# Performance work log

Hardware: AMD Instinct MI355X
Metric: run time of the kernel (lower is better)

## Reference

```python
import jax, jax.numpy as jnp
import numpy as np

H = 4096          # hidden_size
I = 14336         # intermediate_size
G = 128           # quantization group size along the input dim


def dequant(q, s, g=G):
    """Dequantize group-scaled int4 weights.
    q: [out, in] int (values in [-8, 7]); s: [out, in//g] float scales.
    Returns fp weight [out, in]: W[o, i] = q[o, i] * s[o, i // g].
    """
    O, In = q.shape
    return (q.reshape(O, In // g, g).astype(s.dtype) * s[:, :, None]).reshape(O, In)


def setup_inputs() -> dict:
    key = jax.random.key(0)
    ks = jax.random.split(key, 7)
    x = jax.random.normal(ks[0], (2, 2048, H), dtype=jnp.float32)

    def mk_qlinear(kq, ksc, out_d, in_d):
        q = jax.random.randint(kq, (out_d, in_d), -8, 8, dtype=jnp.int32)  # int4 range
        s = jax.random.uniform(ksc, (out_d, in_d // G), dtype=jnp.float32,
                               minval=0.005, maxval=0.02)
        return q, s

    gate_q, gate_s = mk_qlinear(ks[1], ks[2], I, H)
    up_q, up_s = mk_qlinear(ks[3], ks[4], I, H)
    down_q, down_s = mk_qlinear(ks[5], ks[6], H, I)
    return {"x": x,
            "gate_q": gate_q, "gate_s": gate_s,
            "up_q": up_q, "up_s": up_s,
            "down_q": down_q, "down_s": down_s}


def reference(x, gate_q, gate_s, up_q, up_s, down_q, down_s):
    # SwiGLU MLP: down( silu(gate(x)) * up(x) ) with group-dequantized weights.
    Wg = dequant(gate_q, gate_s)   # [I, H]
    Wu = dequant(up_q, up_s)       # [I, H]
    Wd = dequant(down_q, down_s)   # [H, I]
    gate_score = jax.nn.silu(jnp.einsum('bsh,ih->bsi', x, Wg))
    intermediate = gate_score * jnp.einsum('bsh,ih->bsi', x, Wu)
    return jnp.einsum('bsi,hi->bsh', intermediate, Wd)
```

## Files before the change

### kernel.cpp

```cpp
#include <hip/hip_runtime.h>
#include <hip/hip_bf16.h>


#define HDIM 4096
#define IDIM 14336
#define MTOK 4096
#define GRP 128

typedef __attribute__((ext_vector_type(8))) short bf16x8;
typedef __attribute__((ext_vector_type(4))) float f32x4;
typedef __attribute__((ext_vector_type(4))) unsigned short u16x4;

#define WAIT_LGKM0 asm volatile("s_waitcnt lgkmcnt(0)" ::: "memory")
#define WAIT_VM(N) asm volatile("s_waitcnt vmcnt(" #N ")" ::: "memory")
#define SBAR       __builtin_amdgcn_s_barrier()
#define SCHB       __builtin_amdgcn_sched_barrier(0)

__device__ __forceinline__ unsigned short f2bf(float f) {
  union { float f; unsigned int u; } v; v.f = f;
  return (unsigned short)((v.u + 0x7fffu + ((v.u >> 16) & 1u)) >> 16);
}
__device__ __forceinline__ unsigned pk2(float a, float b) {
  union { float f; unsigned u; } ua, ub; ua.f = a; ub.f = b;
  return __builtin_amdgcn_perm(ub.u, ua.u, 0x07060302u);
}

#define GLD16(G, L)                                                           \
  __builtin_amdgcn_global_load_lds(                                           \
      (const __attribute__((address_space(1))) unsigned int*)(G),             \
      (__attribute__((address_space(3))) unsigned int*)(L), 16, 0, 0)

__global__ __launch_bounds__(256) void cvt_x_kernel(const float* __restrict__ x,
                                                    unsigned short* __restrict__ xb) {
  const int n = MTOK * HDIM;
  const int stride = gridDim.x * 256 * 4;
  for (int i = (blockIdx.x * 256 + threadIdx.x) * 4; i < n; i += stride) {
    float4 v = *reinterpret_cast<const float4*>(x + i);
    u16x4 o;
    o[0] = f2bf(v.x); o[1] = f2bf(v.y); o[2] = f2bf(v.z); o[3] = f2bf(v.w);
    *reinterpret_cast<u16x4*>(xb + i) = o;
  }
}

__global__ __launch_bounds__(256) void deq_kernel(const int* __restrict__ q,
                                                  const float* __restrict__ s,
                                                  unsigned short* __restrict__ w,
                                                  int In) {
  const int row  = blockIdx.y;
  const int col0 = blockIdx.x * 2048 + threadIdx.x * 8;
  const long base = (long)row * In + col0;
  const float sc = s[row * (In / GRP) + (col0 >> 7)];
  const int4* p = (const int4*)(q + base);
  int4 a0 = p[0], a1 = p[1];
  uint4 o;
  o.x = pk2((float)a0.x * sc, (float)a0.y * sc);
  o.y = pk2((float)a0.z * sc, (float)a0.w * sc);
  o.z = pk2((float)a1.x * sc, (float)a1.y * sc);
  o.w = pk2((float)a1.z * sc, (float)a1.w * sc);
  *(uint4*)(w + base) = o;
}

__global__ __launch_bounds__(512, 2) void gateup_bf16(
    const unsigned short* __restrict__ xb,
    const unsigned short* __restrict__ wg,
    const unsigned short* __restrict__ wu,
    unsigned short* __restrict__ inter)
{
  __shared__ unsigned short As[2 * 256 * 64];
  __shared__ unsigned short Bgs[2 * 128 * 64];
  __shared__ unsigned short Bus[2 * 128 * 64];

  const int tid = threadIdx.x, lane = tid & 63, wid = tid >> 6;
  const int wm = wid >> 1, wn = wid & 1;
  const int p = blockIdx.x;
  const int l = (p & 7) * 224 + (p >> 3);
  const int m0 = (l & 15) * 256, n0 = (l >> 4) * 128;
  const int lr = lane & 15, lc = lane >> 4;

  const int ra   = tid >> 3;
  const int scol = ((tid & 7) ^ (ra & 7)) << 3;
  const unsigned short* pa  = xb + (long)(m0 + ra) * HDIM + scol;
  const unsigned short* pbg = wg + (long)(n0 + ra) * HDIM + scol;
  const unsigned short* pbu = wu + (long)(n0 + ra) * HDIM + scol;

#define A1(KT, BUF, IT)                                                       \
  GLD16(pa + (long)(IT) * 64 * HDIM + (long)(KT) * 64,                        \
        (unsigned short*)As + (BUF) * 16384 + (IT) * 4096 + wid * 512)
#define BG1(KT, BUF, IT)                                                      \
  GLD16(pbg + (long)(IT) * 64 * HDIM + (long)(KT) * 64,                       \
        (unsigned short*)Bgs + (BUF) * 8192 + (IT) * 4096 + wid * 512)
#define BU1(KT, BUF, IT)                                                      \
  GLD16(pbu + (long)(IT) * 64 * HDIM + (long)(KT) * 64,                       \
        (unsigned short*)Bus + (BUF) * 8192 + (IT) * 4096 + wid * 512)

  f32x4 accg[4][4], accu[4][4];
  const f32x4 zero = {0.f, 0.f, 0.f, 0.f};
#pragma unroll
  for (int i = 0; i < 4; ++i)
#pragma unroll
    for (int j = 0; j < 4; ++j) { accg[i][j] = zero; accu[i][j] = zero; }

  BG1(0, 0, 0); BG1(0, 0, 1); BU1(0, 0, 0); BU1(0, 0, 1);
  A1(0, 0, 0); A1(0, 0, 1); A1(0, 0, 2); A1(0, 0, 3);
  SCHB;
  WAIT_VM(0);
  SBAR;
  SCHB;

  const int NK = HDIM / 64;
#pragma unroll 1
  for (int kt = 0; kt < NK; ++kt) {
    const int RD = kt & 1, WR = RD ^ 1;
    const int ktn = (kt + 1 < NK) ? kt + 1 : NK - 1;
    const unsigned short* Ab  = (const unsigned short*)As  + RD * 16384;
    const unsigned short* Bgb = (const unsigned short*)Bgs + RD * 8192;
    const unsigned short* Bub = (const unsigned short*)Bus + RD * 8192;
    const int soff0 = (lc ^ (lr & 7)) << 3;
    const int soff1 = ((4 + lc) ^ (lr & 7)) << 3;
    bf16x8 af[4], bg[4], bu[4];

#pragma unroll
    for (int mi = 0; mi < 4; ++mi)
      af[mi] = *(const bf16x8*)&Ab[(wm * 64 + mi * 16 + lr) * 64 + soff0];
#pragma unroll
    for (int ni = 0; ni < 4; ++ni) {
      bg[ni] = *(const bf16x8*)&Bgb[(wn * 64 + ni * 16 + lr) * 64 + soff0];
      bu[ni] = *(const bf16x8*)&Bub[(wn * 64 + ni * 16 + lr) * 64 + soff0];
    }
    BG1(ktn, WR, 0); BG1(ktn, WR, 1); BU1(ktn, WR, 0); BU1(ktn, WR, 1);
    SCHB; WAIT_LGKM0; SCHB;
    __builtin_amdgcn_s_setprio(1);
#pragma unroll
    for (int ni = 0; ni < 4; ++ni)
#pragma unroll
      for (int mi = 0; mi < 4; ++mi) {
        accg[mi][ni] = __builtin_amdgcn_mfma_f32_16x16x32_bf16(af[mi], bg[ni], accg[mi][ni], 0, 0, 0);
        accu[mi][ni] = __builtin_amdgcn_mfma_f32_16x16x32_bf16(af[mi], bu[ni], accu[mi][ni], 0, 0, 0);
      }
    __builtin_amdgcn_s_setprio(0);

#pragma unroll
    for (int mi = 0; mi < 4; ++mi)
      af[mi] = *(const bf16x8*)&Ab[(wm * 64 + mi * 16 + lr) * 64 + soff1];
#pragma unroll
    for (int ni = 0; ni < 4; ++ni) {
      bg[ni] = *(const bf16x8*)&Bgb[(wn * 64 + ni * 16 + lr) * 64 + soff1];
      bu[ni] = *(const bf16x8*)&Bub[(wn * 64 + ni * 16 + lr) * 64 + soff1];
    }
    A1(ktn, WR, 0); A1(ktn, WR, 1); A1(ktn, WR, 2); A1(ktn, WR, 3);
    SCHB; WAIT_LGKM0; SCHB;
    __builtin_amdgcn_s_setprio(1);
#pragma unroll
    for (int ni = 0; ni < 4; ++ni)
#pragma unroll
      for (int mi = 0; mi < 4; ++mi) {
        accg[mi][ni] = __builtin_amdgcn_mfma_f32_16x16x32_bf16(af[mi], bg[ni], accg[mi][ni], 0, 0, 0);
        accu[mi][ni] = __builtin_amdgcn_mfma_f32_16x16x32_bf16(af[mi], bu[ni], accu[mi][ni], 0, 0, 0);
      }
    __builtin_amdgcn_s_setprio(0);

    SCHB;
    WAIT_VM(0);
    SBAR;
    SCHB;
  }

  const int r0 = m0 + wm * 64, c0 = n0 + wn * 64;
#pragma unroll
  for (int mi = 0; mi < 4; ++mi)
#pragma unroll
    for (int ni = 0; ni < 4; ++ni)
#pragma unroll
      for (int r = 0; r < 4; ++r) {
        float g = accg[mi][ni][r], u = accu[mi][ni][r];
        float sv = g / (1.f + __expf(-g));
        int row = r0 + mi * 16 + lc * 4 + r;
        int col = c0 + ni * 16 + lr;
        inter[(long)row * IDIM + col] = f2bf(sv * u);
      }
#undef A1
#undef BG1
#undef BU1
}

__global__ __launch_bounds__(512, 2) void down_bf16(
    const unsigned short* __restrict__ inter,
    const unsigned short* __restrict__ wd,
    float* __restrict__ out)
{
  __shared__ unsigned short As[2 * 256 * 64];
  __shared__ unsigned short Bs[2 * 256 * 64];

  const int tid = threadIdx.x, lane = tid & 63, wid = tid >> 6;
  const int wm = wid >> 2, wn = wid & 3;
  const int p = blockIdx.x;
  const int l = (p & 7) * 32 + (p >> 3);
  const int m0 = (l & 15) * 256, n0 = (l >> 4) * 256;
  const int lr = lane & 15, lc = lane >> 4;

  const int ra   = tid >> 3;
  const int scol = ((tid & 7) ^ (ra & 7)) << 3;
  const unsigned short* pa = inter + (long)(m0 + ra) * IDIM + scol;
  const unsigned short* pb = wd + (long)(n0 + ra) * IDIM + scol;

#define DA1(KT, BUF, IT)                                                      \
  GLD16(pa + (long)(IT) * 64 * IDIM + (long)(KT) * 64,                        \
        (unsigned short*)As + (BUF) * 16384 + (IT) * 4096 + wid * 512)
#define DB1(KT, BUF, IT)                                                      \
  GLD16(pb + (long)(IT) * 64 * IDIM + (long)(KT) * 64,                        \
        (unsigned short*)Bs + (BUF) * 16384 + (IT) * 4096 + wid * 512)

  f32x4 acc[8][4];
  const f32x4 zero = {0.f, 0.f, 0.f, 0.f};
#pragma unroll
  for (int i = 0; i < 8; ++i)
#pragma unroll
    for (int j = 0; j < 4; ++j) acc[i][j] = zero;

  DB1(0, 0, 0); DB1(0, 0, 1); DB1(0, 0, 2); DB1(0, 0, 3);
  DA1(0, 0, 0); DA1(0, 0, 1); DA1(0, 0, 2); DA1(0, 0, 3);
  SCHB;
  WAIT_VM(0);
  SBAR;
  SCHB;

  const int NK = IDIM / 64;
#pragma unroll 1
  for (int kt = 0; kt < NK; ++kt) {
    const int RD = kt & 1, WR = RD ^ 1;
    const int ktn = (kt + 1 < NK) ? kt + 1 : NK - 1;
    const unsigned short* Ab = (const unsigned short*)As + RD * 16384;
    const unsigned short* Bb = (const unsigned short*)Bs + RD * 16384;
    const int soff0 = (lc ^ (lr & 7)) << 3;
    const int soff1 = ((4 + lc) ^ (lr & 7)) << 3;
    bf16x8 af[8], bfr[4];

#pragma unroll
    for (int mi = 0; mi < 8; ++mi)
      af[mi] = *(const bf16x8*)&Ab[(wm * 128 + mi * 16 + lr) * 64 + soff0];
#pragma unroll
    for (int ni = 0; ni < 4; ++ni)
      bfr[ni] = *(const bf16x8*)&Bb[(wn * 64 + ni * 16 + lr) * 64 + soff0];
    DB1(ktn, WR, 0); DB1(ktn, WR, 1); DB1(ktn, WR, 2); DB1(ktn, WR, 3);
    SCHB; WAIT_LGKM0; SCHB;
    __builtin_amdgcn_s_setprio(1);
#pragma unroll
    for (int ni = 0; ni < 4; ++ni)
#pragma unroll
      for (int mi = 0; mi < 8; ++mi)
        acc[mi][ni] = __builtin_amdgcn_mfma_f32_16x16x32_bf16(af[mi], bfr[ni], acc[mi][ni], 0, 0, 0);
    __builtin_amdgcn_s_setprio(0);

#pragma unroll
    for (int mi = 0; mi < 8; ++mi)
      af[mi] = *(const bf16x8*)&Ab[(wm * 128 + mi * 16 + lr) * 64 + soff1];
#pragma unroll
    for (int ni = 0; ni < 4; ++ni)
      bfr[ni] = *(const bf16x8*)&Bb[(wn * 64 + ni * 16 + lr) * 64 + soff1];
    DA1(ktn, WR, 0); DA1(ktn, WR, 1); DA1(ktn, WR, 2); DA1(ktn, WR, 3);
    SCHB; WAIT_LGKM0; SCHB;
    __builtin_amdgcn_s_setprio(1);
#pragma unroll
    for (int ni = 0; ni < 4; ++ni)
#pragma unroll
      for (int mi = 0; mi < 8; ++mi)
        acc[mi][ni] = __builtin_amdgcn_mfma_f32_16x16x32_bf16(af[mi], bfr[ni], acc[mi][ni], 0, 0, 0);
    __builtin_amdgcn_s_setprio(0);

    SCHB;
    WAIT_VM(0);
    SBAR;
    SCHB;
  }

  const int r0 = m0 + wm * 128, c0 = n0 + wn * 64;
#pragma unroll
  for (int mi = 0; mi < 8; ++mi)
#pragma unroll
    for (int ni = 0; ni < 4; ++ni)
#pragma unroll
      for (int r = 0; r < 4; ++r) {
        int row = r0 + mi * 16 + lc * 4 + r;
        int col = c0 + ni * 16 + lr;
        out[(long)row * HDIM + col] = acc[mi][ni][r];
      }
#undef DA1
#undef DB1
}

extern "C" void kernel_launch(void* const* d_in, const int* in_sizes, int n_in,
                              void* d_out, int out_size, void* d_ws, size_t ws_size,
                              hipStream_t stream) {
  const float* x   = (const float*)d_in[0];
  const int*   gq  = (const int*)d_in[1];
  const float* gsc = (const float*)d_in[2];
  const int*   uq  = (const int*)d_in[3];
  const float* usc = (const float*)d_in[4];
  const int*   dq  = (const int*)d_in[5];
  const float* dsc = (const float*)d_in[6];
  float* out = (float*)d_out;

  unsigned short* xb    = (unsigned short*)d_ws;
  unsigned short* inter = xb + (size_t)MTOK * HDIM;
  unsigned short* wgb   = inter + (size_t)MTOK * IDIM;
  unsigned short* wub   = wgb + (size_t)IDIM * HDIM;

  hipLaunchKernelGGL(cvt_x_kernel, dim3(2048), dim3(256), 0, stream, x, xb);
  hipLaunchKernelGGL(deq_kernel, dim3(HDIM / 2048, IDIM), dim3(256), 0, stream,
                     gq, gsc, wgb, HDIM);
  hipLaunchKernelGGL(deq_kernel, dim3(HDIM / 2048, IDIM), dim3(256), 0, stream,
                     uq, usc, wub, HDIM);
  hipLaunchKernelGGL(gateup_bf16, dim3(1792), dim3(512), 0, stream,
                     xb, wgb, wub, inter);
  hipLaunchKernelGGL(deq_kernel, dim3(IDIM / 2048, HDIM), dim3(256), 0, stream,
                     dq, dsc, wgb, IDIM);
  hipLaunchKernelGGL(down_bf16, dim3(256), dim3(512), 0, stream,
                     inter, wgb, out);
}
```

Measured before the change: 1.387 ms.

## Fold down-proj dequant into gate/up GEMM launch as extra blocks

Adds 256 extra blocks to the gate/up GEMM grid that dequantize the down-projection weights into a separate workspace buffer, then return. This removes a separate dequant launch and lets the dequant traffic overlap with GEMM compute. It needs more workspace, and falls back to the old path if the workspace is too small. The dequant blocks are scheduled first and occupy CUs that the GEMM tiles would otherwise use.

```diff
diff --git a/kernel.cpp b/kernel.cpp
--- a/kernel.cpp
+++ b/kernel.cpp
@@ -64,15 +64,37 @@
     const unsigned short* __restrict__ xb,
     const unsigned short* __restrict__ wg,
     const unsigned short* __restrict__ wu,
-    unsigned short* __restrict__ inter)
+    unsigned short* __restrict__ inter,
+    const int* __restrict__ dnq, const float* __restrict__ dns,
+    unsigned short* __restrict__ wdb, int nDeq)
 {
   __shared__ unsigned short As[2 * 256 * 64];
   __shared__ unsigned short Bgs[2 * 128 * 64];
   __shared__ unsigned short Bus[2 * 128 * 64];
 
+  if ((int)blockIdx.x < nDeq) {
+    const long total = (long)HDIM * (IDIM / 8);
+    const long stride = (long)nDeq * 512;
+    for (long idx = (long)blockIdx.x * 512 + threadIdx.x; idx < total; idx += stride) {
+      const long e = idx * 8;
+      const int row = (int)(e / IDIM);
+      const int col = (int)(e - (long)row * IDIM);
+      const float sc = dns[row * (IDIM / GRP) + (col >> 7)];
+      const int4* q4 = (const int4*)(dnq + (long)row * IDIM + col);
+      int4 a0 = q4[0], a1 = q4[1];
+      uint4 o;
+      o.x = pk2((float)a0.x * sc, (float)a0.y * sc);
+      o.y = pk2((float)a0.z * sc, (float)a0.w * sc);
+      o.z = pk2((float)a1.x * sc, (float)a1.y * sc);
+      o.w = pk2((float)a1.z * sc, (float)a1.w * sc);
+      *(uint4*)(wdb + (long)row * IDIM + col) = o;
+    }
+    return;
+  }
+
   const int tid = threadIdx.x, lane = tid & 63, wid = tid >> 6;
   const int wm = wid >> 1, wn = wid & 1;
-  const int p = blockIdx.x;
+  const int p = (int)blockIdx.x - nDeq;
   const int l = (p & 7) * 224 + (p >> 3);
   const int m0 = (l & 15) * 256, n0 = (l >> 4) * 128;
   const int lr = lane & 15, lc = lane >> 4;
@@ -304,16 +326,27 @@
   unsigned short* inter = xb + (size_t)MTOK * HDIM;
   unsigned short* wgb   = inter + (size_t)MTOK * IDIM;
   unsigned short* wub   = wgb + (size_t)IDIM * HDIM;
+  unsigned short* wdb   = wub + (size_t)IDIM * HDIM;
+  const size_t needOverlap = ((size_t)MTOK * HDIM + (size_t)MTOK * IDIM +
+                              3 * (size_t)IDIM * HDIM) * 2;
 
   hipLaunchKernelGGL(cvt_x_kernel, dim3(2048), dim3(256), 0, stream, x, xb);
   hipLaunchKernelGGL(deq_kernel, dim3(HDIM / 2048, IDIM), dim3(256), 0, stream,
                      gq, gsc, wgb, HDIM);
   hipLaunchKernelGGL(deq_kernel, dim3(HDIM / 2048, IDIM), dim3(256), 0, stream,
                      uq, usc, wub, HDIM);
-  hipLaunchKernelGGL(gateup_bf16, dim3(1792), dim3(512), 0, stream,
-                     xb, wgb, wub, inter);
-  hipLaunchKernelGGL(deq_kernel, dim3(IDIM / 2048, HDIM), dim3(256), 0, stream,
-                     dq, dsc, wgb, IDIM);
-  hipLaunchKernelGGL(down_bf16, dim3(256), dim3(512), 0, stream,
-                     inter, wgb, out);
-}
+
+  if (ws_size >= needOverlap) {
+    hipLaunchKernelGGL(gateup_bf16, dim3(256 + 1792), dim3(512), 0, stream,
+                       xb, wgb, wub, inter, dq, dsc, wdb, 256);
+    hipLaunchKernelGGL(down_bf16, dim3(256), dim3(512), 0, stream,
+                       inter, wdb, out);
+  } else {
+    hipLaunchKernelGGL(gateup_bf16, dim3(1792), dim3(512), 0, stream,
+                       xb, wgb, wub, inter, dq, dsc, wgb, 0);
+    hipLaunchKernelGGL(deq_kernel, dim3(IDIM / 2048, HDIM), dim3(256), 0, stream,
+                       dq, dsc, wgb, IDIM);
+    hipLaunchKernelGGL(down_bf16, dim3(256), dim3(512), 0, stream,
+                       inter, wgb, out);
+  }
+}
```

Measured after the change: 1.374 ms, median of 3. Within noise of the previous version (-1.0%).
